# Kernel tuning notes

Measured on AMD Instinct MI355X. Metric: run time of the kernel, lower is better.

Reference implementation:

```python
import jax, jax.numpy as jnp
import numpy as np

STALK_DIM = 16
N_NODES = 50000
N_EDGES = 400000
HIDDEN = 64


def setup_inputs() -> dict:
    key = jax.random.key(0)
    k1, k2, k3, k4 = jax.random.split(key, 4)
    d = STALK_DIM
    x = jax.random.normal(k1, (N_NODES, d), dtype=jnp.float32)
    edge_index = jax.random.randint(k2, (2, N_EDGES), 0, N_NODES, dtype=jnp.int64)
    W1 = jax.random.normal(k3, (HIDDEN, 2 * d), dtype=jnp.float32) * (1.0 / np.sqrt(2 * d))
    b1 = jnp.zeros((HIDDEN,), dtype=jnp.float32)
    W2 = jax.random.normal(k4, (d, HIDDEN), dtype=jnp.float32) * (1.0 / np.sqrt(HIDDEN))
    b2 = jnp.zeros((d,), dtype=jnp.float32)
    return {"x": x, "edge_index": edge_index, "W1": W1, "b1": b1, "W2": W2, "b2": b2}


def reference(x, edge_index, W1, b1, W2, b2):
    d = x.shape[1]
    n = x.shape[0]
    src, dst = edge_index[0], edge_index[1]
    xs, xd = x[src], x[dst]  # [E, d]

    def reflection(a, b):
        h = jax.nn.relu(jnp.concatenate([a, b], axis=1) @ W1.T + b1)
        return h @ W2.T + b2  # [E, d]

    def householder(v):
        # F.normalize(v, dim=1): v / max(||v||, 1e-12)
        vn = v / jnp.maximum(jnp.linalg.norm(v, axis=1, keepdims=True), 1e-12)
        return jnp.eye(d, dtype=v.dtype)[None] - 2.0 * vn[:, :, None] * vn[:, None, :]

    F_s = householder(reflection(xs, xd))  # [E, d, d]
    F_d = householder(reflection(xd, xs))  # [E, d, d]
    L_sd = -jnp.einsum('eki,ekj->eij', F_s, F_d)  # -F_s^T @ F_d, [E, d, d]

    # degrees: both endpoints of every edge contribute 1
    ones_e = jnp.ones(src.shape[0], dtype=x.dtype)
    deg = jnp.zeros(n, dtype=x.dtype).at[src].add(ones_e).at[dst].add(ones_e)
    deg_inv_sqrt = 1.0 / jnp.sqrt(jnp.maximum(deg, 1e-5))
    # D_inv_sqrt is scalar*I per node, so normalization is a scalar coefficient per edge
    coef = deg_inv_sqrt[src] * deg_inv_sqrt[dst]  # [E]

    # out[s] -= D^-1/2_s L D^-1/2_d x[d] ; out[d] -= D^-1/2_d L^T D^-1/2_s x[s]
    msg_s = coef[:, None] * jnp.einsum('eij,ej->ei', L_sd, xd)  # goes to src
    msg_d = coef[:, None] * jnp.einsum('eji,ej->ei', L_sd, xs)  # goes to dst

    out = x - jnp.zeros_like(x).at[src].add(msg_s) - jnp.zeros_like(x).at[dst].add(msg_d)
    return jax.nn.relu(out)
```

## Files before the change

kernel.cpp:

```cpp
#include <hip/hip_runtime.h>
#include <hip/hip_bf16.h>
#include <hip/hip_fp16.h>

#define N_NODES 50000
#define N_EDGES 400000
#define D 16
#define HID 64

#define SCAN_B 256
#define SCAN_G ((N_NODES + SCAN_B - 1) / SCAN_B)

typedef unsigned short ushort_t;
typedef _Float16 h16x2 __attribute__((ext_vector_type(2)));

#define CNT4_OFF  0
#define DEG_OFF   (4 * N_NODES)
#define OFF_OFF   (5 * N_NODES)
#define CUR_OFF   (6 * N_NODES + 1)
#define BS_OFF    (7 * N_NODES + 1)
#define MSG_OFF_I (((BS_OFF + SCAN_G) + 3) & ~3)
#define CSR_NEEDED_BYTES ((size_t)(MSG_OFF_I + 2 * N_EDGES * D) * 4 + 64)

#define FB_NDEG   (N_NODES)
#define FB_NACC   (N_NODES * D)
#define FB_FLAGS  (FB_NDEG + FB_NACC)

__device__ __forceinline__ float bf_bits(ushort_t us) {
    return __uint_as_float(((unsigned)us) << 16);
}
__device__ __forceinline__ float lo_bf(unsigned u) { return __uint_as_float(u << 16); }
__device__ __forceinline__ float hi_bf(unsigned u) { return __uint_as_float(u & 0xffff0000u); }
__device__ __forceinline__ ushort_t f2bf(float v) {
    unsigned u = __float_as_uint(v);
    unsigned r = (u + 0x7fffu + ((u >> 16) & 1u)) >> 16;
    return (ushort_t)r;
}
__device__ __forceinline__ float ld_f(const void* p, int idx, int f32) {
    return f32 ? ((const float*)p)[idx]
               : bf_bits(((const ushort_t*)p)[idx]);
}

__device__ __forceinline__ unsigned pack_h2(float a, float b) {
#if __has_builtin(__builtin_amdgcn_cvt_pkrtz)
    return __builtin_bit_cast(unsigned, __builtin_amdgcn_cvt_pkrtz(a, b));
#else
    h16x2 h;
    h.x = (_Float16)a;
    h.y = (_Float16)b;
    return __builtin_bit_cast(unsigned, h);
#endif
}

#if __has_builtin(__builtin_amdgcn_fdot2)
__device__ __forceinline__ float fdot2u(unsigned a, unsigned b, float c) {
    return __builtin_amdgcn_fdot2(__builtin_bit_cast(h16x2, a),
                                  __builtin_bit_cast(h16x2, b), c, false);
}
#else
__device__ __forceinline__ float fdot2u(unsigned a, unsigned b, float c) {
    h16x2 ha = __builtin_bit_cast(h16x2, a);
    h16x2 hb = __builtin_bit_cast(h16x2, b);
    return fmaf((float)ha.x, (float)hb.x, fmaf((float)ha.y, (float)hb.y, c));
}
#endif

__device__ __forceinline__ void ld16u(const unsigned* __restrict__ p, unsigned* o) {
    const uint4* q = (const uint4*)p;
    uint4 a = q[0], b = q[1], c = q[2], d = q[3];
    o[0]=a.x; o[1]=a.y; o[2]=a.z; o[3]=a.w;
    o[4]=b.x; o[5]=b.y; o[6]=b.z; o[7]=b.w;
    o[8]=c.x; o[9]=c.y; o[10]=c.z; o[11]=c.w;
    o[12]=d.x; o[13]=d.y; o[14]=d.z; o[15]=d.w;
}

__device__ __forceinline__ void load16(const void* __restrict__ p, long long base,
                                       int f32, float* o) {
    if (f32) {
        const float4* q = (const float4*)((const float*)p + base);
        float4 a = q[0], b = q[1], c = q[2], d = q[3];
        o[0]=a.x; o[1]=a.y; o[2]=a.z; o[3]=a.w;
        o[4]=b.x; o[5]=b.y; o[6]=b.z; o[7]=b.w;
        o[8]=c.x; o[9]=c.y; o[10]=c.z; o[11]=c.w;
        o[12]=d.x; o[13]=d.y; o[14]=d.z; o[15]=d.w;
    } else {
        const uint4* q = (const uint4*)((const ushort_t*)p + base);
        uint4 a = q[0], b = q[1];
        unsigned u[8] = {a.x, a.y, a.z, a.w, b.x, b.y, b.z, b.w};
#pragma unroll
        for (int k = 0; k < 8; k++) {
            o[2 * k]     = lo_bf(u[k]);
            o[2 * k + 1] = hi_bf(u[k]);
        }
    }
}

__device__ __forceinline__ void load_edge(const void* __restrict__ ei, int e, int is64,
                                          int& s, int& d) {
    if (is64) {
        const long long* p = (const long long*)ei;
        s = (int)p[e];
        d = (int)p[N_EDGES + e];
    } else {
        const int* p = (const int*)ei;
        s = p[e];
        d = p[N_EDGES + e];
    }
}

__device__ __forceinline__ void detect_flags(const void* x, const void* ei, int* flags) {
    const ushort_t* h = (const ushort_t*)x;
    int f32 = 0;
    for (int k = 0; k < 256; k++) {
        float v = bf_bits(h[k]);
        if (!(v == v) || fabsf(v) > 1.0e6f) { f32 = 1; break; }
    }
    const long long* p = (const long long*)ei;
    int i64 = 1;
    for (int k = 0; k < 16; k++) {
        long long v = p[k];
        if (v < 0 || v >= N_NODES) { i64 = 0; break; }
    }
    flags[0] = f32;
    flags[1] = i64;
}

__device__ __forceinline__ void stage_weights(
    const void* W1, const void* b1, const void* W2, const void* b2, int f32,
    float* sW1, float* sW2t, float* sb1, float* sb2)
{
    int t = threadIdx.x;
    for (int idx = t; idx < HID * 2 * D; idx += blockDim.x)
        sW1[idx] = ld_f(W1, idx, f32);
    for (int idx = t; idx < HID * D; idx += blockDim.x) {
        int j = idx / D, i = idx % D;
        sW2t[idx] = ld_f(W2, i * HID + j, f32);
    }
    if (t < HID) sb1[t] = ld_f(b1, t, f32);
    if (t < D)  sb2[t] = ld_f(b2, t, f32);
}

__device__ __forceinline__ void edge_math_v4(
    const float* __restrict__ sW1, const float* __restrict__ sW2t,
    const float* __restrict__ sb1, const float* __restrict__ sb2,
    const float* xs, const float* xd, float coef,
    float* ms, float* md)
{
    float vs[D], vd[D];
#pragma unroll
    for (int i = 0; i < D; i++) { vs[i] = sb2[i]; vd[i] = sb2[i]; }
#pragma unroll 4
    for (int j = 0; j < HID; j++) {
        float hs = sb1[j], hd = sb1[j];
        const float4* w4 = (const float4*)&sW1[j * 2 * D];
#pragma unroll
        for (int t = 0; t < 4; t++) {
            float4 wv = w4[t];
            int k = 4 * t;
            hs = fmaf(wv.x, xs[k],     hs); hd = fmaf(wv.x, xd[k],     hd);
            hs = fmaf(wv.y, xs[k + 1], hs); hd = fmaf(wv.y, xd[k + 1], hd);
            hs = fmaf(wv.z, xs[k + 2], hs); hd = fmaf(wv.z, xd[k + 2], hd);
            hs = fmaf(wv.w, xs[k + 3], hs); hd = fmaf(wv.w, xd[k + 3], hd);
        }
#pragma unroll
        for (int t = 0; t < 4; t++) {
            float4 wv = w4[4 + t];
            int k = 4 * t;
            hs = fmaf(wv.x, xd[k],     hs); hd = fmaf(wv.x, xs[k],     hd);
            hs = fmaf(wv.y, xd[k + 1], hs); hd = fmaf(wv.y, xs[k + 1], hd);
            hs = fmaf(wv.z, xd[k + 2], hs); hd = fmaf(wv.z, xs[k + 2], hd);
            hs = fmaf(wv.w, xd[k + 3], hs); hd = fmaf(wv.w, xs[k + 3], hd);
        }
        hs = fmaxf(hs, 0.0f);
        hd = fmaxf(hd, 0.0f);
        const float4* w24 = (const float4*)&sW2t[j * D];
#pragma unroll
        for (int t = 0; t < 4; t++) {
            float4 u = w24[t];
            int i = 4 * t;
            vs[i]     = fmaf(u.x, hs, vs[i]);     vd[i]     = fmaf(u.x, hd, vd[i]);
            vs[i + 1] = fmaf(u.y, hs, vs[i + 1]); vd[i + 1] = fmaf(u.y, hd, vd[i + 1]);
            vs[i + 2] = fmaf(u.z, hs, vs[i + 2]); vd[i + 2] = fmaf(u.z, hd, vd[i + 2]);
            vs[i + 3] = fmaf(u.w, hs, vs[i + 3]); vd[i + 3] = fmaf(u.w, hd, vd[i + 3]);
        }
    }
    float ns = 0.0f, nd = 0.0f;
#pragma unroll
    for (int i = 0; i < D; i++) { ns = fmaf(vs[i], vs[i], ns); nd = fmaf(vd[i], vd[i], nd); }
    float is_ = 1.0f / fmaxf(sqrtf(ns), 1e-12f);
    float id_ = 1.0f / fmaxf(sqrtf(nd), 1e-12f);
#pragma unroll
    for (int i = 0; i < D; i++) { vs[i] *= is_; vd[i] *= id_; }
    float dot1 = 0.0f;
#pragma unroll
    for (int i = 0; i < D; i++) dot1 = fmaf(vd[i], xd[i], dot1);
#pragma unroll
    for (int i = 0; i < D; i++) ms[i] = fmaf(-2.0f * dot1, vd[i], xd[i]);
    float dot2 = 0.0f;
#pragma unroll
    for (int i = 0; i < D; i++) dot2 = fmaf(vs[i], ms[i], dot2);
#pragma unroll
    for (int i = 0; i < D; i++) ms[i] = coef * fmaf(-2.0f * dot2, vs[i], ms[i]);
    float dot3 = 0.0f;
#pragma unroll
    for (int i = 0; i < D; i++) dot3 = fmaf(vs[i], xs[i], dot3);
#pragma unroll
    for (int i = 0; i < D; i++) md[i] = fmaf(-2.0f * dot3, vs[i], xs[i]);
    float dot4 = 0.0f;
#pragma unroll
    for (int i = 0; i < D; i++) dot4 = fmaf(vd[i], md[i], dot4);
#pragma unroll
    for (int i = 0; i < D; i++) md[i] = coef * fmaf(-2.0f * dot4, vd[i], md[i]);
}

__global__ void csr_count_kernel(const void* __restrict__ ei,
                                 const void* __restrict__ x,
                                 int* __restrict__ wsI) {
    __shared__ int sfl[2];
    if (threadIdx.x == 0) detect_flags(x, ei, sfl);
    __syncthreads();
    int i64 = sfl[1];
    int e = blockIdx.x * blockDim.x + threadIdx.x;
    if (e >= N_EDGES) return;
    int s, d;
    load_edge(ei, e, i64, s, d);
    int r = (e & 3) * N_NODES;
    atomicAdd(&wsI[CNT4_OFF + r + s], 1);
    atomicAdd(&wsI[CNT4_OFF + r + d], 1);
}

__global__ __launch_bounds__(SCAN_B) void csr_scan1_kernel(int* __restrict__ wsI) {
    __shared__ int sm[SCAN_B];
    int t = threadIdx.x;
    int g = blockIdx.x * SCAN_B + t;
    int c = 0;
    if (g < N_NODES) {
        c = wsI[CNT4_OFF + g] + wsI[CNT4_OFF + N_NODES + g]
          + wsI[CNT4_OFF + 2 * N_NODES + g] + wsI[CNT4_OFF + 3 * N_NODES + g];
        wsI[DEG_OFF + g] = c;
    }
    sm[t] = c;
    __syncthreads();
    for (int st = SCAN_B / 2; st > 0; st >>= 1) {
        if (t < st) sm[t] += sm[t + st];
        __syncthreads();
    }
    if (t == 0) wsI[BS_OFF + blockIdx.x] = sm[0];
}

__global__ __launch_bounds__(SCAN_B) void csr_scan3_kernel(int* __restrict__ wsI) {
    __shared__ int sB[SCAN_B];
    __shared__ int sm[SCAN_B];
    int t = threadIdx.x;
    int bsv = (t < SCAN_G) ? wsI[BS_OFF + t] : 0;
    sB[t] = bsv;
    __syncthreads();
    for (int st = 1; st < SCAN_B; st <<= 1) {
        int u = (t >= st) ? sB[t - st] : 0;
        __syncthreads();
        sB[t] += u;
        __syncthreads();
    }
    int blockBase = sB[blockIdx.x] - wsI[BS_OFF + blockIdx.x];

    int g = blockIdx.x * SCAN_B + t;
    int c = (g < N_NODES) ? wsI[DEG_OFF + g] : 0;
    sm[t] = c;
    __syncthreads();
    for (int st = 1; st < SCAN_B; st <<= 1) {
        int u = (t >= st) ? sm[t - st] : 0;
        __syncthreads();
        sm[t] += u;
        __syncthreads();
    }
    int excl = sm[t] - c + blockBase;
    if (g < N_NODES) {
        wsI[OFF_OFF + g] = excl;
        wsI[CUR_OFF + g] = excl;
        if (g == N_NODES - 1) wsI[OFF_OFF + N_NODES] = excl + c;
    }
}

__global__ __launch_bounds__(256) void csr_edge_kernel(
    const void* __restrict__ x,
    const void* __restrict__ ei,
    const void* __restrict__ W1,
    const void* __restrict__ b1,
    const void* __restrict__ W2,
    const void* __restrict__ b2,
    int* __restrict__ wsI)
{
    __shared__ __align__(16) unsigned sW1h[HID * 16];
    __shared__ __align__(16) unsigned sW2h[32 * 16];
    __shared__ float sb1[HID];
    __shared__ float sb2[D];
    __shared__ __align__(16) float sW1f[HID * 2 * D];
    __shared__ __align__(16) float sW2tf[HID * D];
    __shared__ int sfl[2];

    if (threadIdx.x == 0) detect_flags(x, ei, sfl);
    __syncthreads();
    int f32 = sfl[0], i64 = sfl[1];
    int t = threadIdx.x;

    if (!f32) {
        const ushort_t* W1b = (const ushort_t*)W1;
        for (int idx = t; idx < HID * 16; idx += 256) {
            int j = idx >> 4, tt = idx & 15;
            sW1h[idx] = pack_h2(bf_bits(W1b[j * 32 + 2 * tt]),
                                bf_bits(W1b[j * 32 + 2 * tt + 1]));
        }
        const ushort_t* W2b = (const ushort_t*)W2;
        for (int idx = t; idx < 32 * 16; idx += 256) {
            int jj = idx >> 4, i = idx & 15;
            sW2h[idx] = pack_h2(bf_bits(W2b[i * HID + 2 * jj]),
                                bf_bits(W2b[i * HID + 2 * jj + 1]));
        }
    } else {
        for (int idx = t; idx < HID * 2 * D; idx += 256)
            sW1f[idx] = ld_f(W1, idx, 1);
        for (int idx = t; idx < HID * D; idx += 256) {
            int j = idx / D, i = idx % D;
            sW2tf[idx] = ld_f(W2, i * HID + j, 1);
        }
    }
    if (t < HID) sb1[t] = ld_f(b1, t, f32);
    if (t < D)  sb2[t] = ld_f(b2, t, f32);
    __syncthreads();

    int e = blockIdx.x * 256 + t;
    if (e >= N_EDGES) return;

    int s, d;
    load_edge(ei, e, i64, s, d);
    float degs = (float)wsI[DEG_OFF + s];
    float degd = (float)wsI[DEG_OFF + d];
    float coef = (1.0f / sqrtf(fmaxf(degs, 1e-5f))) * (1.0f / sqrtf(fmaxf(degd, 1e-5f)));
    float* msg = (float*)(wsI + MSG_OFF_I);

    if (!f32) {
        unsigned xsh[8], xdh[8];
        {
            const uint4* q = (const uint4*)((const ushort_t*)x + (long long)s * D);
            uint4 a = q[0], b = q[1];
            unsigned u[8] = {a.x, a.y, a.z, a.w, b.x, b.y, b.z, b.w};
#pragma unroll
            for (int k = 0; k < 8; k++) xsh[k] = pack_h2(lo_bf(u[k]), hi_bf(u[k]));
        }
        {
            const uint4* q = (const uint4*)((const ushort_t*)x + (long long)d * D);
            uint4 a = q[0], b = q[1];
            unsigned u[8] = {a.x, a.y, a.z, a.w, b.x, b.y, b.z, b.w};
#pragma unroll
            for (int k = 0; k < 8; k++) xdh[k] = pack_h2(lo_bf(u[k]), hi_bf(u[k]));
        }

        float vs[D], vd[D];
#pragma unroll
        for (int i = 0; i < D; i++) { vs[i] = sb2[i]; vd[i] = sb2[i]; }

#pragma unroll 2
        for (int jj = 0; jj < 32; jj++) {
            unsigned wr[32];
            ld16u(&sW1h[(2 * jj) * 16], wr);
            ld16u(&sW1h[(2 * jj) * 16 + 16], wr + 16);
            unsigned w2r[16];
            ld16u(&sW2h[jj * 16], w2r);

            float hs0 = sb1[2 * jj],     hd0 = hs0;
            float hs1 = sb1[2 * jj + 1], hd1 = hs1;
#pragma unroll
            for (int k = 0; k < 8; k++) {
                hs0 = fdot2u(wr[k],      xsh[k], hs0);
                hd0 = fdot2u(wr[k],      xdh[k], hd0);
                hs1 = fdot2u(wr[16 + k], xsh[k], hs1);
                hd1 = fdot2u(wr[16 + k], xdh[k], hd1);
            }
#pragma unroll
            for (int k = 0; k < 8; k++) {
                hs0 = fdot2u(wr[8 + k],  xdh[k], hs0);
                hd0 = fdot2u(wr[8 + k],  xsh[k], hd0);
                hs1 = fdot2u(wr[24 + k], xdh[k], hs1);
                hd1 = fdot2u(wr[24 + k], xsh[k], hd1);
            }
            hs0 = fmaxf(hs0, 0.0f); hd0 = fmaxf(hd0, 0.0f);
            hs1 = fmaxf(hs1, 0.0f); hd1 = fmaxf(hd1, 0.0f);
            unsigned hsp = pack_h2(hs0, hs1);
            unsigned hdp = pack_h2(hd0, hd1);
#pragma unroll
            for (int i = 0; i < D; i++) {
                vs[i] = fdot2u(w2r[i], hsp, vs[i]);
                vd[i] = fdot2u(w2r[i], hdp, vd[i]);
            }
        }

        float xs[D], xd[D];
#pragma unroll
        for (int k = 0; k < 8; k++) {
            h16x2 a = __builtin_bit_cast(h16x2, xsh[k]);
            xs[2 * k] = (float)a.x; xs[2 * k + 1] = (float)a.y;
            h16x2 b = __builtin_bit_cast(h16x2, xdh[k]);
            xd[2 * k] = (float)b.x; xd[2 * k + 1] = (float)b.y;
        }

        float ns = 0.0f, nd = 0.0f;
#pragma unroll
        for (int i = 0; i < D; i++) { ns = fmaf(vs[i], vs[i], ns); nd = fmaf(vd[i], vd[i], nd); }
        float is_ = 1.0f / fmaxf(sqrtf(ns), 1e-12f);
        float id_ = 1.0f / fmaxf(sqrtf(nd), 1e-12f);
#pragma unroll
        for (int i = 0; i < D; i++) { vs[i] *= is_; vd[i] *= id_; }

        float ms[D], md[D];
        float dot1 = 0.0f;
#pragma unroll
        for (int i = 0; i < D; i++) dot1 = fmaf(vd[i], xd[i], dot1);
#pragma unroll
        for (int i = 0; i < D; i++) ms[i] = fmaf(-2.0f * dot1, vd[i], xd[i]);
        float dot2 = 0.0f;
#pragma unroll
        for (int i = 0; i < D; i++) dot2 = fmaf(vs[i], ms[i], dot2);
#pragma unroll
        for (int i = 0; i < D; i++) ms[i] = coef * fmaf(-2.0f * dot2, vs[i], ms[i]);
        float dot3 = 0.0f;
#pragma unroll
        for (int i = 0; i < D; i++) dot3 = fmaf(vs[i], xs[i], dot3);
#pragma unroll
        for (int i = 0; i < D; i++) md[i] = fmaf(-2.0f * dot3, vs[i], xs[i]);
        float dot4 = 0.0f;
#pragma unroll
        for (int i = 0; i < D; i++) dot4 = fmaf(vd[i], md[i], dot4);
#pragma unroll
        for (int i = 0; i < D; i++) md[i] = coef * fmaf(-2.0f * dot4, vd[i], md[i]);

        int slot_s = atomicAdd(&wsI[CUR_OFF + s], 1);
        float4* m0 = (float4*)(msg + (long long)slot_s * D);
        m0[0] = make_float4(ms[0], ms[1], ms[2], ms[3]);
        m0[1] = make_float4(ms[4], ms[5], ms[6], ms[7]);
        m0[2] = make_float4(ms[8], ms[9], ms[10], ms[11]);
        m0[3] = make_float4(ms[12], ms[13], ms[14], ms[15]);
        int slot_d = atomicAdd(&wsI[CUR_OFF + d], 1);
        float4* m1 = (float4*)(msg + (long long)slot_d * D);
        m1[0] = make_float4(md[0], md[1], md[2], md[3]);
        m1[1] = make_float4(md[4], md[5], md[6], md[7]);
        m1[2] = make_float4(md[8], md[9], md[10], md[11]);
        m1[3] = make_float4(md[12], md[13], md[14], md[15]);
    } else {
        float xs[D], xd[D];
        load16(x, (long long)s * D, 1, xs);
        load16(x, (long long)d * D, 1, xd);
        float ms[D], md[D];
        edge_math_v4(sW1f, sW2tf, sb1, sb2, xs, xd, coef, ms, md);
        int slot_s = atomicAdd(&wsI[CUR_OFF + s], 1);
        float4* m0 = (float4*)(msg + (long long)slot_s * D);
        m0[0] = make_float4(ms[0], ms[1], ms[2], ms[3]);
        m0[1] = make_float4(ms[4], ms[5], ms[6], ms[7]);
        m0[2] = make_float4(ms[8], ms[9], ms[10], ms[11]);
        m0[3] = make_float4(ms[12], ms[13], ms[14], ms[15]);
        int slot_d = atomicAdd(&wsI[CUR_OFF + d], 1);
        float4* m1 = (float4*)(msg + (long long)slot_d * D);
        m1[0] = make_float4(md[0], md[1], md[2], md[3]);
        m1[1] = make_float4(md[4], md[5], md[6], md[7]);
        m1[2] = make_float4(md[8], md[9], md[10], md[11]);
        m1[3] = make_float4(md[12], md[13], md[14], md[15]);
    }
}

__global__ __launch_bounds__(256) void csr_gather_kernel(
    const void* __restrict__ x,
    const void* __restrict__ ei,
    const int* __restrict__ wsI,
    void* __restrict__ out)
{
    __shared__ int sfl[2];
    if (threadIdx.x == 0) detect_flags(x, ei, sfl);
    __syncthreads();
    int f32 = sfl[0];

    int n = blockIdx.x * 64 + (threadIdx.x >> 2);
    int c = threadIdx.x & 3;
    if (n >= N_NODES) return;

    const int* off = wsI + OFF_OFF;
    const float4* msg4 = (const float4*)(wsI + MSG_OFF_I);

    int beg = off[n], end = off[n + 1];
    float4 a = make_float4(0.0f, 0.0f, 0.0f, 0.0f);
    int it = beg;
    for (; it + 2 <= end; it += 2) {
        float4 u = msg4[(long long)it * 4 + c];
        float4 v = msg4[(long long)(it + 1) * 4 + c];
        a.x += u.x + v.x; a.y += u.y + v.y; a.z += u.z + v.z; a.w += u.w + v.w;
    }
    if (it < end) {
        float4 u = msg4[(long long)it * 4 + c];
        a.x += u.x; a.y += u.y; a.z += u.z; a.w += u.w;
    }

    long long xb = (long long)n * D + 4 * c;
    float4 xv;
    if (f32) {
        xv = *(const float4*)((const float*)x + xb);
    } else {
        uint2 u = *(const uint2*)((const ushort_t*)x + xb);
        xv.x = lo_bf(u.x); xv.y = hi_bf(u.x);
        xv.z = lo_bf(u.y); xv.w = hi_bf(u.y);
    }
    float4 r;
    r.x = fmaxf(xv.x + a.x, 0.0f);
    r.y = fmaxf(xv.y + a.y, 0.0f);
    r.z = fmaxf(xv.z + a.z, 0.0f);
    r.w = fmaxf(xv.w + a.w, 0.0f);
    if (f32) {
        *(float4*)((float*)out + xb) = r;
    } else {
        uint2 o;
        o.x = (unsigned)f2bf(r.x) | ((unsigned)f2bf(r.y) << 16);
        o.y = (unsigned)f2bf(r.z) | ((unsigned)f2bf(r.w) << 16);
        *(uint2*)((ushort_t*)out + xb) = o;
    }
}

__global__ void fb_init_kernel(float* __restrict__ ws,
                               const void* __restrict__ x,
                               const void* __restrict__ ei) {
    int i = blockIdx.x * blockDim.x + threadIdx.x;
    if (i < FB_FLAGS) ws[i] = 0.0f;
    if (blockIdx.x == 0 && threadIdx.x == 0)
        detect_flags(x, ei, (int*)(ws + FB_FLAGS));
}

__global__ void fb_deg_kernel(const void* __restrict__ ei, float* __restrict__ ws) {
    int i64 = ((const int*)(ws + FB_FLAGS))[1];
    int e = blockIdx.x * blockDim.x + threadIdx.x;
    if (e >= N_EDGES) return;
    int s, d;
    load_edge(ei, e, i64, s, d);
    atomicAdd(&ws[s], 1.0f);
    atomicAdd(&ws[d], 1.0f);
}

__global__ __launch_bounds__(256) void fb_edge_kernel(
    const void* __restrict__ x, const void* __restrict__ ei,
    const void* __restrict__ W1, const void* __restrict__ b1,
    const void* __restrict__ W2, const void* __restrict__ b2,
    float* __restrict__ ws)
{
    __shared__ __align__(16) float sW1[HID * 2 * D];
    __shared__ __align__(16) float sW2t[HID * D];
    __shared__ float sb1[HID];
    __shared__ float sb2[D];
    const int* flags = (const int*)(ws + FB_FLAGS);
    int f32 = flags[0], i64 = flags[1];
    stage_weights(W1, b1, W2, b2, f32, sW1, sW2t, sb1, sb2);
    __syncthreads();
    int e = blockIdx.x * blockDim.x + threadIdx.x;
    if (e >= N_EDGES) return;
    int s, d;
    load_edge(ei, e, i64, s, d);
    float xs[D], xd[D];
    load16(x, (long long)s * D, f32, xs);
    load16(x, (long long)d * D, f32, xd);
    float coef = (1.0f / sqrtf(fmaxf(ws[s], 1e-5f))) * (1.0f / sqrtf(fmaxf(ws[d], 1e-5f)));
    float ms[D], md[D];
    edge_math_v4(sW1, sW2t, sb1, sb2, xs, xd, coef, ms, md);
    float* acc = ws + FB_NDEG;
#pragma unroll
    for (int i = 0; i < D; i++) atomicAdd(&acc[(long long)s * D + i], ms[i]);
#pragma unroll
    for (int i = 0; i < D; i++) atomicAdd(&acc[(long long)d * D + i], md[i]);
}

__global__ void fb_finalize_kernel(const void* __restrict__ x,
                                   const float* __restrict__ ws,
                                   void* __restrict__ out)
{
    int f32 = ((const int*)(ws + FB_FLAGS))[0];
    const float* acc = ws + FB_NDEG;
    int i = blockIdx.x * blockDim.x + threadIdx.x;
    if (i >= FB_NACC) return;
    float v = ld_f(x, i, f32) + acc[i];
    v = fmaxf(v, 0.0f);
    if (f32) ((float*)out)[i] = v;
    else     ((__hip_bfloat16*)out)[i] = __float2bfloat16(v);
}

extern "C" void kernel_launch(void* const* d_in, const int* in_sizes, int n_in,
                              void* d_out, int out_size, void* d_ws, size_t ws_size,
                              hipStream_t stream)
{
    const void* x  = d_in[0];
    const void* ei = d_in[1];
    const void* W1 = d_in[2];
    const void* b1 = d_in[3];
    const void* W2 = d_in[4];
    const void* b2 = d_in[5];

    int blk = 256;
    if (ws_size >= CSR_NEEDED_BYTES) {
        int* wsI = (int*)d_ws;
        hipMemsetAsync(d_ws, 0, (size_t)4 * N_NODES * sizeof(int), stream);
        csr_count_kernel<<<(N_EDGES + blk - 1) / blk, blk, 0, stream>>>(ei, x, wsI);
        csr_scan1_kernel<<<SCAN_G, SCAN_B, 0, stream>>>(wsI);
        csr_scan3_kernel<<<SCAN_G, SCAN_B, 0, stream>>>(wsI);
        csr_edge_kernel<<<(N_EDGES + blk - 1) / blk, blk, 0, stream>>>(x, ei, W1, b1, W2, b2, wsI);
        csr_gather_kernel<<<(N_NODES + 63) / 64, blk, 0, stream>>>(x, ei, wsI, d_out);
    } else {
        float* ws = (float*)d_ws;
        fb_init_kernel<<<(FB_FLAGS + blk - 1) / blk, blk, 0, stream>>>(ws, x, ei);
        fb_deg_kernel<<<(N_EDGES + blk - 1) / blk, blk, 0, stream>>>(ei, ws);
        fb_edge_kernel<<<(N_EDGES + blk - 1) / blk, blk, 0, stream>>>(x, ei, W1, b1, W2, b2, ws);
        fb_finalize_kernel<<<(FB_NACC + blk - 1) / blk, blk, 0, stream>>>(x, ws, d_out);
    }
}
```

Before: 200.0 us.

## Compute per-edge MLP with MFMA matrix instructions in bf16 path

Replaces the per-thread fdot2-based two-layer MLP in the bf16 path with wave-level MFMA: each wave processes 64 edges in 16-edge groups, computing hidden activations with bf16 MFMA and the output layer with f16 MFMA via an LDS staging buffer. Weights are held in registers per lane instead of shared memory. The Householder math and message scatter stay per-thread, reading MLP outputs back from LDS. This adds LDS traffic and precision changes (bf16 first layer inputs) in exchange for much higher arithmetic throughput.

```diff
diff --git a/kernel.cpp b/kernel.cpp
--- a/kernel.cpp
+++ b/kernel.cpp
@@ -12,6 +12,9 @@
 
 typedef unsigned short ushort_t;
 typedef _Float16 h16x2 __attribute__((ext_vector_type(2)));
+typedef __attribute__((ext_vector_type(8))) short bf16x8_t;
+typedef __attribute__((ext_vector_type(8))) _Float16 f16x8_t;
+typedef __attribute__((ext_vector_type(4))) float f32x4_t;
 
 #define CNT4_OFF  0
 #define DEG_OFF   (4 * N_NODES)
@@ -24,6 +27,12 @@
 #define FB_NDEG   (N_NODES)
 #define FB_NACC   (N_NODES * D)
 #define FB_FLAGS  (FB_NDEG + FB_NACC)
+
+#define HSTRIDE 80
+#define VSTRIDE 36
+#define WAVE_H_BYTES (16 * HSTRIDE * 2)
+#define WAVE_V_BYTES (64 * VSTRIDE * 4)
+#define WAVE_LDS (WAVE_H_BYTES + WAVE_V_BYTES)
 
 __device__ __forceinline__ float bf_bits(ushort_t us) {
     return __uint_as_float(((unsigned)us) << 16);
@@ -49,28 +58,6 @@
     h.y = (_Float16)b;
     return __builtin_bit_cast(unsigned, h);
 #endif
-}
-
-#if __has_builtin(__builtin_amdgcn_fdot2)
-__device__ __forceinline__ float fdot2u(unsigned a, unsigned b, float c) {
-    return __builtin_amdgcn_fdot2(__builtin_bit_cast(h16x2, a),
-                                  __builtin_bit_cast(h16x2, b), c, false);
-}
-#else
-__device__ __forceinline__ float fdot2u(unsigned a, unsigned b, float c) {
-    h16x2 ha = __builtin_bit_cast(h16x2, a);
-    h16x2 hb = __builtin_bit_cast(h16x2, b);
-    return fmaf((float)ha.x, (float)hb.x, fmaf((float)ha.y, (float)hb.y, c));
-}
-#endif
-
-__device__ __forceinline__ void ld16u(const unsigned* __restrict__ p, unsigned* o) {
-    const uint4* q = (const uint4*)p;
-    uint4 a = q[0], b = q[1], c = q[2], d = q[3];
-    o[0]=a.x; o[1]=a.y; o[2]=a.z; o[3]=a.w;
-    o[4]=b.x; o[5]=b.y; o[6]=b.z; o[7]=b.w;
-    o[8]=c.x; o[9]=c.y; o[10]=c.z; o[11]=c.w;
-    o[12]=d.x; o[13]=d.y; o[14]=d.z; o[15]=d.w;
 }
 
 __device__ __forceinline__ void load16(const void* __restrict__ p, long long base,
@@ -289,162 +276,36 @@
     const void* __restrict__ b2,
     int* __restrict__ wsI)
 {
-    __shared__ __align__(16) unsigned sW1h[HID * 16];
-    __shared__ __align__(16) unsigned sW2h[32 * 16];
-    __shared__ float sb1[HID];
-    __shared__ float sb2[D];
-    __shared__ __align__(16) float sW1f[HID * 2 * D];
-    __shared__ __align__(16) float sW2tf[HID * D];
+    __shared__ __align__(16) char smem[4 * WAVE_LDS];
     __shared__ int sfl[2];
-
     if (threadIdx.x == 0) detect_flags(x, ei, sfl);
     __syncthreads();
     int f32 = sfl[0], i64 = sfl[1];
     int t = threadIdx.x;
-
-    if (!f32) {
-        const ushort_t* W1b = (const ushort_t*)W1;
-        for (int idx = t; idx < HID * 16; idx += 256) {
-            int j = idx >> 4, tt = idx & 15;
-            sW1h[idx] = pack_h2(bf_bits(W1b[j * 32 + 2 * tt]),
-                                bf_bits(W1b[j * 32 + 2 * tt + 1]));
-        }
-        const ushort_t* W2b = (const ushort_t*)W2;
-        for (int idx = t; idx < 32 * 16; idx += 256) {
-            int jj = idx >> 4, i = idx & 15;
-            sW2h[idx] = pack_h2(bf_bits(W2b[i * HID + 2 * jj]),
-                                bf_bits(W2b[i * HID + 2 * jj + 1]));
-        }
-    } else {
+    float* msg = (float*)(wsI + MSG_OFF_I);
+
+    if (f32) {
+        float* sW1f  = (float*)smem;
+        float* sW2tf = sW1f + HID * 2 * D;
+        float* sb1   = sW2tf + HID * D;
+        float* sb2   = sb1 + HID;
         for (int idx = t; idx < HID * 2 * D; idx += 256)
-            sW1f[idx] = ld_f(W1, idx, 1);
+            sW1f[idx] = ((const float*)W1)[idx];
         for (int idx = t; idx < HID * D; idx += 256) {
             int j = idx / D, i = idx % D;
-            sW2tf[idx] = ld_f(W2, i * HID + j, 1);
-        }
-    }
-    if (t < HID) sb1[t] = ld_f(b1, t, f32);
-    if (t < D)  sb2[t] = ld_f(b2, t, f32);
-    __syncthreads();
-
-    int e = blockIdx.x * 256 + t;
-    if (e >= N_EDGES) return;
-
-    int s, d;
-    load_edge(ei, e, i64, s, d);
-    float degs = (float)wsI[DEG_OFF + s];
-    float degd = (float)wsI[DEG_OFF + d];
-    float coef = (1.0f / sqrtf(fmaxf(degs, 1e-5f))) * (1.0f / sqrtf(fmaxf(degd, 1e-5f)));
-    float* msg = (float*)(wsI + MSG_OFF_I);
-
-    if (!f32) {
-        unsigned xsh[8], xdh[8];
-        {
-            const uint4* q = (const uint4*)((const ushort_t*)x + (long long)s * D);
-            uint4 a = q[0], b = q[1];
-            unsigned u[8] = {a.x, a.y, a.z, a.w, b.x, b.y, b.z, b.w};
-#pragma unroll
-            for (int k = 0; k < 8; k++) xsh[k] = pack_h2(lo_bf(u[k]), hi_bf(u[k]));
-        }
-        {
-            const uint4* q = (const uint4*)((const ushort_t*)x + (long long)d * D);
-            uint4 a = q[0], b = q[1];
-            unsigned u[8] = {a.x, a.y, a.z, a.w, b.x, b.y, b.z, b.w};
-#pragma unroll
-            for (int k = 0; k < 8; k++) xdh[k] = pack_h2(lo_bf(u[k]), hi_bf(u[k]));
-        }
-
-        float vs[D], vd[D];
-#pragma unroll
-        for (int i = 0; i < D; i++) { vs[i] = sb2[i]; vd[i] = sb2[i]; }
-
-#pragma unroll 2
-        for (int jj = 0; jj < 32; jj++) {
-            unsigned wr[32];
-            ld16u(&sW1h[(2 * jj) * 16], wr);
-            ld16u(&sW1h[(2 * jj) * 16 + 16], wr + 16);
-            unsigned w2r[16];
-            ld16u(&sW2h[jj * 16], w2r);
-
-            float hs0 = sb1[2 * jj],     hd0 = hs0;
-            float hs1 = sb1[2 * jj + 1], hd1 = hs1;
-#pragma unroll
-            for (int k = 0; k < 8; k++) {
-                hs0 = fdot2u(wr[k],      xsh[k], hs0);
-                hd0 = fdot2u(wr[k],      xdh[k], hd0);
-                hs1 = fdot2u(wr[16 + k], xsh[k], hs1);
-                hd1 = fdot2u(wr[16 + k], xdh[k], hd1);
-            }
-#pragma unroll
-            for (int k = 0; k < 8; k++) {
-                hs0 = fdot2u(wr[8 + k],  xdh[k], hs0);
-                hd0 = fdot2u(wr[8 + k],  xsh[k], hd0);
-                hs1 = fdot2u(wr[24 + k], xdh[k], hs1);
-                hd1 = fdot2u(wr[24 + k], xsh[k], hd1);
-            }
-            hs0 = fmaxf(hs0, 0.0f); hd0 = fmaxf(hd0, 0.0f);
-            hs1 = fmaxf(hs1, 0.0f); hd1 = fmaxf(hd1, 0.0f);
-            unsigned hsp = pack_h2(hs0, hs1);
-            unsigned hdp = pack_h2(hd0, hd1);
-#pragma unroll
-            for (int i = 0; i < D; i++) {
-                vs[i] = fdot2u(w2r[i], hsp, vs[i]);
-                vd[i] = fdot2u(w2r[i], hdp, vd[i]);
-            }
-        }
-
-        float xs[D], xd[D];
-#pragma unroll
-        for (int k = 0; k < 8; k++) {
-            h16x2 a = __builtin_bit_cast(h16x2, xsh[k]);
-            xs[2 * k] = (float)a.x; xs[2 * k + 1] = (float)a.y;
-            h16x2 b = __builtin_bit_cast(h16x2, xdh[k]);
-            xd[2 * k] = (float)b.x; xd[2 * k + 1] = (float)b.y;
-        }
-
-        float ns = 0.0f, nd = 0.0f;
-#pragma unroll
-        for (int i = 0; i < D; i++) { ns = fmaf(vs[i], vs[i], ns); nd = fmaf(vd[i], vd[i], nd); }
-        float is_ = 1.0f / fmaxf(sqrtf(ns), 1e-12f);
-        float id_ = 1.0f / fmaxf(sqrtf(nd), 1e-12f);
-#pragma unroll
-        for (int i = 0; i < D; i++) { vs[i] *= is_; vd[i] *= id_; }
-
-        float ms[D], md[D];
-        float dot1 = 0.0f;
-#pragma unroll
-        for (int i = 0; i < D; i++) dot1 = fmaf(vd[i], xd[i], dot1);
-#pragma unroll
-        for (int i = 0; i < D; i++) ms[i] = fmaf(-2.0f * dot1, vd[i], xd[i]);
-        float dot2 = 0.0f;
-#pragma unroll
-        for (int i = 0; i < D; i++) dot2 = fmaf(vs[i], ms[i], dot2);
-#pragma unroll
-        for (int i = 0; i < D; i++) ms[i] = coef * fmaf(-2.0f * dot2, vs[i], ms[i]);
-        float dot3 = 0.0f;
-#pragma unroll
-        for (int i = 0; i < D; i++) dot3 = fmaf(vs[i], xs[i], dot3);
-#pragma unroll
-        for (int i = 0; i < D; i++) md[i] = fmaf(-2.0f * dot3, vs[i], xs[i]);
-        float dot4 = 0.0f;
-#pragma unroll
-        for (int i = 0; i < D; i++) dot4 = fmaf(vd[i], md[i], dot4);
-#pragma unroll
-        for (int i = 0; i < D; i++) md[i] = coef * fmaf(-2.0f * dot4, vd[i], md[i]);
-
-        int slot_s = atomicAdd(&wsI[CUR_OFF + s], 1);
-        float4* m0 = (float4*)(msg + (long long)slot_s * D);
-        m0[0] = make_float4(ms[0], ms[1], ms[2], ms[3]);
-        m0[1] = make_float4(ms[4], ms[5], ms[6], ms[7]);
-        m0[2] = make_float4(ms[8], ms[9], ms[10], ms[11]);
-        m0[3] = make_float4(ms[12], ms[13], ms[14], ms[15]);
-        int slot_d = atomicAdd(&wsI[CUR_OFF + d], 1);
-        float4* m1 = (float4*)(msg + (long long)slot_d * D);
-        m1[0] = make_float4(md[0], md[1], md[2], md[3]);
-        m1[1] = make_float4(md[4], md[5], md[6], md[7]);
-        m1[2] = make_float4(md[8], md[9], md[10], md[11]);
-        m1[3] = make_float4(md[12], md[13], md[14], md[15]);
-    } else {
+            sW2tf[idx] = ((const float*)W2)[i * HID + j];
+        }
+        if (t < HID) sb1[t] = ((const float*)b1)[t];
+        if (t < D)  sb2[t] = ((const float*)b2)[t];
+        __syncthreads();
+
+        int e = blockIdx.x * 256 + t;
+        if (e >= N_EDGES) return;
+        int s, d;
+        load_edge(ei, e, i64, s, d);
+        float degs = (float)wsI[DEG_OFF + s];
+        float degd = (float)wsI[DEG_OFF + d];
+        float coef = (1.0f / sqrtf(fmaxf(degs, 1e-5f))) * (1.0f / sqrtf(fmaxf(degd, 1e-5f)));
         float xs[D], xd[D];
         load16(x, (long long)s * D, 1, xs);
         load16(x, (long long)d * D, 1, xd);
@@ -462,7 +323,169 @@
         m1[1] = make_float4(md[4], md[5], md[6], md[7]);
         m1[2] = make_float4(md[8], md[9], md[10], md[11]);
         m1[3] = make_float4(md[12], md[13], md[14], md[15]);
-    }
+        return;
+    }
+
+    const int wave = t >> 6;
+    const int lane = t & 63;
+    const int g4 = lane >> 4;
+    const int c  = lane & 15;
+    const int ebase = blockIdx.x * 256 + wave * 64;
+    if (ebase >= N_EDGES) return;
+
+    char* wbase = smem + wave * WAVE_LDS;
+    _Float16* hw = (_Float16*)wbase;
+    float* vbuf = (float*)(wbase + WAVE_H_BYTES);
+
+    const ushort_t* xb  = (const ushort_t*)x;
+    const ushort_t* W1b = (const ushort_t*)W1;
+    const ushort_t* W2b = (const ushort_t*)W2;
+    const ushort_t* b1b = (const ushort_t*)b1;
+    const ushort_t* b2b = (const ushort_t*)b2;
+
+    bf16x8_t B1[4], B1s[4];
+#pragma unroll
+    for (int tt = 0; tt < 4; tt++) {
+        B1[tt]  = *(const bf16x8_t*)(W1b + (16 * tt + c) * (2 * D) + g4 * 8);
+        B1s[tt] = *(const bf16x8_t*)(W1b + (16 * tt + c) * (2 * D) + ((g4 ^ 2) * 8));
+    }
+    f16x8_t B2[2];
+#pragma unroll
+    for (int q = 0; q < 2; q++) {
+        const ushort_t* p = W2b + c * HID + q * 32 + g4 * 8;
+        uint4 raw = *(const uint4*)p;
+        unsigned u[4] = {raw.x, raw.y, raw.z, raw.w};
+        f16x8_t hv;
+#pragma unroll
+        for (int k = 0; k < 4; k++) {
+            hv[2 * k]     = (_Float16)lo_bf(u[k]);
+            hv[2 * k + 1] = (_Float16)hi_bf(u[k]);
+        }
+        B2[q] = hv;
+    }
+    float b1c[4];
+#pragma unroll
+    for (int tt = 0; tt < 4; tt++) b1c[tt] = bf_bits(b1b[16 * tt + c]);
+    float b2c = bf_bits(b2b[c]);
+
+#pragma unroll 1
+    for (int G = 0; G < 4; G++) {
+        const int e0 = ebase + G * 16;
+        int nid = 0;
+        if (lane < 32) {
+            int idx = (lane < 16) ? (e0 + lane) : (N_EDGES + e0 + lane - 16);
+            nid = i64 ? (int)((const long long*)ei)[idx] : ((const int*)ei)[idx];
+        }
+        int an = __shfl(nid, (g4 < 2) ? c : (c + 16), 64);
+        bf16x8_t A1 = *(const bf16x8_t*)(xb + (long long)an * D + (g4 & 1) * 8);
+
+        f32x4_t cs[4], cd[4];
+#pragma unroll
+        for (int tt = 0; tt < 4; tt++) {
+            f32x4_t bi = {b1c[tt], b1c[tt], b1c[tt], b1c[tt]};
+            cs[tt] = __builtin_amdgcn_mfma_f32_16x16x32_bf16(A1, B1[tt],  bi, 0, 0, 0);
+            cd[tt] = __builtin_amdgcn_mfma_f32_16x16x32_bf16(A1, B1s[tt], bi, 0, 0, 0);
+        }
+
+#pragma unroll
+        for (int tt = 0; tt < 4; tt++)
+#pragma unroll
+            for (int r = 0; r < 4; r++)
+                hw[(g4 * 4 + r) * HSTRIDE + 16 * tt + c] = (_Float16)fmaxf(cs[tt][r], 0.0f);
+        f32x4_t vS = {b2c, b2c, b2c, b2c};
+#pragma unroll
+        for (int q = 0; q < 2; q++) {
+            f16x8_t a2 = *(const f16x8_t*)(hw + c * HSTRIDE + q * 32 + g4 * 8);
+            vS = __builtin_amdgcn_mfma_f32_16x16x32_f16(a2, B2[q], vS, 0, 0, 0);
+        }
+#pragma unroll
+        for (int r = 0; r < 4; r++)
+            vbuf[(G * 16 + g4 * 4 + r) * VSTRIDE + c] = vS[r];
+
+#pragma unroll
+        for (int tt = 0; tt < 4; tt++)
+#pragma unroll
+            for (int r = 0; r < 4; r++)
+                hw[(g4 * 4 + r) * HSTRIDE + 16 * tt + c] = (_Float16)fmaxf(cd[tt][r], 0.0f);
+        f32x4_t vD = {b2c, b2c, b2c, b2c};
+#pragma unroll
+        for (int q = 0; q < 2; q++) {
+            f16x8_t a2 = *(const f16x8_t*)(hw + c * HSTRIDE + q * 32 + g4 * 8);
+            vD = __builtin_amdgcn_mfma_f32_16x16x32_f16(a2, B2[q], vD, 0, 0, 0);
+        }
+#pragma unroll
+        for (int r = 0; r < 4; r++)
+            vbuf[(G * 16 + g4 * 4 + r) * VSTRIDE + 16 + c] = vD[r];
+    }
+
+    int e = ebase + lane;
+    int s, d;
+    load_edge(ei, e, i64, s, d);
+    float degs = (float)wsI[DEG_OFF + s];
+    float degd = (float)wsI[DEG_OFF + d];
+    float coef = (1.0f / sqrtf(fmaxf(degs, 1e-5f))) * (1.0f / sqrtf(fmaxf(degd, 1e-5f)));
+
+    float vs[D], vd[D];
+    {
+        const f32x4_t* vp = (const f32x4_t*)(vbuf + lane * VSTRIDE);
+#pragma unroll
+        for (int i = 0; i < 4; i++) {
+            f32x4_t u = vp[i];
+            vs[4 * i] = u[0]; vs[4 * i + 1] = u[1]; vs[4 * i + 2] = u[2]; vs[4 * i + 3] = u[3];
+        }
+        const f32x4_t* vq = (const f32x4_t*)(vbuf + lane * VSTRIDE + 16);
+#pragma unroll
+        for (int i = 0; i < 4; i++) {
+            f32x4_t u = vq[i];
+            vd[4 * i] = u[0]; vd[4 * i + 1] = u[1]; vd[4 * i + 2] = u[2]; vd[4 * i + 3] = u[3];
+        }
+    }
+    float xs[D], xd[D];
+    load16(x, (long long)s * D, 0, xs);
+    load16(x, (long long)d * D, 0, xd);
+
+    float ns = 0.0f, nd = 0.0f;
+#pragma unroll
+    for (int i = 0; i < D; i++) { ns = fmaf(vs[i], vs[i], ns); nd = fmaf(vd[i], vd[i], nd); }
+    float is_ = 1.0f / fmaxf(sqrtf(ns), 1e-12f);
+    float id_ = 1.0f / fmaxf(sqrtf(nd), 1e-12f);
+#pragma unroll
+    for (int i = 0; i < D; i++) { vs[i] *= is_; vd[i] *= id_; }
+
+    float ms[D], md[D];
+    float dot1 = 0.0f;
+#pragma unroll
+    for (int i = 0; i < D; i++) dot1 = fmaf(vd[i], xd[i], dot1);
+#pragma unroll
+    for (int i = 0; i < D; i++) ms[i] = fmaf(-2.0f * dot1, vd[i], xd[i]);
+    float dot2 = 0.0f;
+#pragma unroll
+    for (int i = 0; i < D; i++) dot2 = fmaf(vs[i], ms[i], dot2);
+#pragma unroll
+    for (int i = 0; i < D; i++) ms[i] = coef * fmaf(-2.0f * dot2, vs[i], ms[i]);
+    float dot3 = 0.0f;
+#pragma unroll
+    for (int i = 0; i < D; i++) dot3 = fmaf(vs[i], xs[i], dot3);
+#pragma unroll
+    for (int i = 0; i < D; i++) md[i] = fmaf(-2.0f * dot3, vs[i], xs[i]);
+    float dot4 = 0.0f;
+#pragma unroll
+    for (int i = 0; i < D; i++) dot4 = fmaf(vd[i], md[i], dot4);
+#pragma unroll
+    for (int i = 0; i < D; i++) md[i] = coef * fmaf(-2.0f * dot4, vd[i], md[i]);
+
+    int slot_s = atomicAdd(&wsI[CUR_OFF + s], 1);
+    float4* m0 = (float4*)(msg + (long long)slot_s * D);
+    m0[0] = make_float4(ms[0], ms[1], ms[2], ms[3]);
+    m0[1] = make_float4(ms[4], ms[5], ms[6], ms[7]);
+    m0[2] = make_float4(ms[8], ms[9], ms[10], ms[11]);
+    m0[3] = make_float4(ms[12], ms[13], ms[14], ms[15]);
+    int slot_d = atomicAdd(&wsI[CUR_OFF + d], 1);
+    float4* m1 = (float4*)(msg + (long long)slot_d * D);
+    m1[0] = make_float4(md[0], md[1], md[2], md[3]);
+    m1[1] = make_float4(md[4], md[5], md[6], md[7]);
+    m1[2] = make_float4(md[8], md[9], md[10], md[11]);
+    m1[3] = make_float4(md[12], md[13], md[14], md[15]);
 }
 
 __global__ __launch_bounds__(256) void csr_gather_kernel(
```

After: 220.8 us. 1.1x slower.

## Prepack bf16 weights once in count kernel, read from global in edge kernel

Applied to the files above, without the earlier changes.

Block 0 of the count kernel now converts W1, W2, b1 and b2 from bf16 into packed fp16 pairs and fp32 biases, laid out per hidden pair, and writes them to a workspace region. The edge kernel's bf16 path no longer stages weights into shared memory per block and skips the __syncthreads, loading each 52-dword chunk straight from global/L2 as uniform vector loads with unroll 1. This removes per-block conversion and LDS traffic, and the smaller LDS footprint may raise occupancy, at the cost of global loads in the inner loop. The f32 path is unchanged.

```diff
diff --git a/kernel.cpp b/kernel.cpp
--- a/kernel.cpp
+++ b/kernel.cpp
@@ -19,7 +19,9 @@
 #define CUR_OFF   (6 * N_NODES + 1)
 #define BS_OFF    (7 * N_NODES + 1)
 #define MSG_OFF_I (((BS_OFF + SCAN_G) + 3) & ~3)
-#define CSR_NEEDED_BYTES ((size_t)(MSG_OFF_I + 2 * N_EDGES * D) * 4 + 64)
+#define PREP_OFF  (MSG_OFF_I + 2 * N_EDGES * D)
+#define PREP_DW   (32 * 52 + 16)
+#define CSR_NEEDED_BYTES ((size_t)(PREP_OFF + PREP_DW) * 4 + 64)
 
 #define FB_NDEG   (N_NODES)
 #define FB_NACC   (N_NODES * D)
@@ -63,15 +65,6 @@
     return fmaf((float)ha.x, (float)hb.x, fmaf((float)ha.y, (float)hb.y, c));
 }
 #endif
-
-__device__ __forceinline__ void ld16u(const unsigned* __restrict__ p, unsigned* o) {
-    const uint4* q = (const uint4*)p;
-    uint4 a = q[0], b = q[1], c = q[2], d = q[3];
-    o[0]=a.x; o[1]=a.y; o[2]=a.z; o[3]=a.w;
-    o[4]=b.x; o[5]=b.y; o[6]=b.z; o[7]=b.w;
-    o[8]=c.x; o[9]=c.y; o[10]=c.z; o[11]=c.w;
-    o[12]=d.x; o[13]=d.y; o[14]=d.z; o[15]=d.w;
-}
 
 __device__ __forceinline__ void load16(const void* __restrict__ p, long long base,
                                        int f32, float* o) {
@@ -214,11 +207,44 @@
 
 __global__ void csr_count_kernel(const void* __restrict__ ei,
                                  const void* __restrict__ x,
+                                 const void* __restrict__ W1,
+                                 const void* __restrict__ b1,
+                                 const void* __restrict__ W2,
+                                 const void* __restrict__ b2,
                                  int* __restrict__ wsI) {
     __shared__ int sfl[2];
     if (threadIdx.x == 0) detect_flags(x, ei, sfl);
     __syncthreads();
     int i64 = sfl[1];
+
+    if (blockIdx.x == 0) {
+        unsigned* pp = (unsigned*)(wsI + PREP_OFF);
+        const ushort_t* W1b = (const ushort_t*)W1;
+        const ushort_t* W2b = (const ushort_t*)W2;
+        const ushort_t* b1b = (const ushort_t*)b1;
+        const ushort_t* b2b = (const ushort_t*)b2;
+        for (int idx = threadIdx.x; idx < 32 * 52; idx += 256) {
+            int jj = idx / 52, w = idx % 52;
+            unsigned val = 0;
+            if (w < 32) {
+                int row = 2 * jj + (w >> 4), k2 = w & 15;
+                val = pack_h2(bf_bits(W1b[row * 32 + 2 * k2]),
+                              bf_bits(W1b[row * 32 + 2 * k2 + 1]));
+            } else if (w < 48) {
+                int i = w - 32;
+                val = pack_h2(bf_bits(W2b[i * HID + 2 * jj]),
+                              bf_bits(W2b[i * HID + 2 * jj + 1]));
+            } else if (w == 48) {
+                val = __float_as_uint(bf_bits(b1b[2 * jj]));
+            } else if (w == 49) {
+                val = __float_as_uint(bf_bits(b1b[2 * jj + 1]));
+            }
+            pp[idx] = val;
+        }
+        if (threadIdx.x < D)
+            pp[32 * 52 + threadIdx.x] = __float_as_uint(bf_bits(b2b[threadIdx.x]));
+    }
+
     int e = blockIdx.x * blockDim.x + threadIdx.x;
     if (e >= N_EDGES) return;
     int s, d;
@@ -287,14 +313,13 @@
     const void* __restrict__ b1,
     const void* __restrict__ W2,
     const void* __restrict__ b2,
+    const unsigned* __restrict__ prep,
     int* __restrict__ wsI)
 {
-    __shared__ __align__(16) unsigned sW1h[HID * 16];
-    __shared__ __align__(16) unsigned sW2h[32 * 16];
+    __shared__ __align__(16) float sW1f[HID * 2 * D];
+    __shared__ __align__(16) float sW2tf[HID * D];
     __shared__ float sb1[HID];
     __shared__ float sb2[D];
-    __shared__ __align__(16) float sW1f[HID * 2 * D];
-    __shared__ __align__(16) float sW2tf[HID * D];
     __shared__ int sfl[2];
 
     if (threadIdx.x == 0) detect_flags(x, ei, sfl);
@@ -302,30 +327,17 @@
     int f32 = sfl[0], i64 = sfl[1];
     int t = threadIdx.x;
 
-    if (!f32) {
-        const ushort_t* W1b = (const ushort_t*)W1;
-        for (int idx = t; idx < HID * 16; idx += 256) {
-            int j = idx >> 4, tt = idx & 15;
-            sW1h[idx] = pack_h2(bf_bits(W1b[j * 32 + 2 * tt]),
-                                bf_bits(W1b[j * 32 + 2 * tt + 1]));
-        }
-        const ushort_t* W2b = (const ushort_t*)W2;
-        for (int idx = t; idx < 32 * 16; idx += 256) {
-            int jj = idx >> 4, i = idx & 15;
-            sW2h[idx] = pack_h2(bf_bits(W2b[i * HID + 2 * jj]),
-                                bf_bits(W2b[i * HID + 2 * jj + 1]));
-        }
-    } else {
+    if (f32) {
         for (int idx = t; idx < HID * 2 * D; idx += 256)
             sW1f[idx] = ld_f(W1, idx, 1);
         for (int idx = t; idx < HID * D; idx += 256) {
             int j = idx / D, i = idx % D;
             sW2tf[idx] = ld_f(W2, i * HID + j, 1);
         }
-    }
-    if (t < HID) sb1[t] = ld_f(b1, t, f32);
-    if (t < D)  sb2[t] = ld_f(b2, t, f32);
-    __syncthreads();
+        if (t < HID) sb1[t] = ld_f(b1, t, 1);
+        if (t < D)  sb2[t] = ld_f(b2, t, 1);
+        __syncthreads();
+    }
 
     int e = blockIdx.x * 256 + t;
     if (e >= N_EDGES) return;
@@ -354,33 +366,40 @@
             for (int k = 0; k < 8; k++) xdh[k] = pack_h2(lo_bf(u[k]), hi_bf(u[k]));
         }
 
+        const float* b2f = (const float*)(prep + 32 * 52);
         float vs[D], vd[D];
 #pragma unroll
-        for (int i = 0; i < D; i++) { vs[i] = sb2[i]; vd[i] = sb2[i]; }
-
-#pragma unroll 2
+        for (int i = 0; i < D; i++) { vs[i] = b2f[i]; vd[i] = b2f[i]; }
+
+#pragma unroll 1
         for (int jj = 0; jj < 32; jj++) {
-            unsigned wr[32];
-            ld16u(&sW1h[(2 * jj) * 16], wr);
-            ld16u(&sW1h[(2 * jj) * 16 + 16], wr + 16);
-            unsigned w2r[16];
-            ld16u(&sW2h[jj * 16], w2r);
-
-            float hs0 = sb1[2 * jj],     hd0 = hs0;
-            float hs1 = sb1[2 * jj + 1], hd1 = hs1;
+            const uint4* wb = (const uint4*)(prep + jj * 52);
+            uint4 q0 = wb[0], q1 = wb[1], q2 = wb[2], q3 = wb[3];
+            uint4 q4 = wb[4], q5 = wb[5], q6 = wb[6], q7 = wb[7];
+            uint4 q8 = wb[8], q9 = wb[9], qA = wb[10], qB = wb[11];
+            const float* bb = (const float*)(prep + jj * 52 + 48);
+            float hs0 = bb[0], hd0 = bb[0];
+            float hs1 = bb[1], hd1 = bb[1];
+
+            unsigned r0[16] = {q0.x, q0.y, q0.z, q0.w, q1.x, q1.y, q1.z, q1.w,
+                               q2.x, q2.y, q2.z, q2.w, q3.x, q3.y, q3.z, q3.w};
+            unsigned r1[16] = {q4.x, q4.y, q4.z, q4.w, q5.x, q5.y, q5.z, q5.w,
+                               q6.x, q6.y, q6.z, q6.w, q7.x, q7.y, q7.z, q7.w};
+            unsigned w2a[16] = {q8.x, q8.y, q8.z, q8.w, q9.x, q9.y, q9.z, q9.w,
+                                qA.x, qA.y, qA.z, qA.w, qB.x, qB.y, qB.z, qB.w};
 #pragma unroll
             for (int k = 0; k < 8; k++) {
-                hs0 = fdot2u(wr[k],      xsh[k], hs0);
-                hd0 = fdot2u(wr[k],      xdh[k], hd0);
-                hs1 = fdot2u(wr[16 + k], xsh[k], hs1);
-                hd1 = fdot2u(wr[16 + k], xdh[k], hd1);
+                hs0 = fdot2u(r0[k], xsh[k], hs0);
+                hd0 = fdot2u(r0[k], xdh[k], hd0);
+                hs1 = fdot2u(r1[k], xsh[k], hs1);
+                hd1 = fdot2u(r1[k], xdh[k], hd1);
             }
 #pragma unroll
             for (int k = 0; k < 8; k++) {
-                hs0 = fdot2u(wr[8 + k],  xdh[k], hs0);
-                hd0 = fdot2u(wr[8 + k],  xsh[k], hd0);
-                hs1 = fdot2u(wr[24 + k], xdh[k], hs1);
-                hd1 = fdot2u(wr[24 + k], xsh[k], hd1);
+                hs0 = fdot2u(r0[8 + k], xdh[k], hs0);
+                hd0 = fdot2u(r0[8 + k], xsh[k], hd0);
+                hs1 = fdot2u(r1[8 + k], xdh[k], hs1);
+                hd1 = fdot2u(r1[8 + k], xsh[k], hd1);
             }
             hs0 = fmaxf(hs0, 0.0f); hd0 = fmaxf(hd0, 0.0f);
             hs1 = fmaxf(hs1, 0.0f); hd1 = fmaxf(hd1, 0.0f);
@@ -388,8 +407,8 @@
             unsigned hdp = pack_h2(hd0, hd1);
 #pragma unroll
             for (int i = 0; i < D; i++) {
-                vs[i] = fdot2u(w2r[i], hsp, vs[i]);
-                vd[i] = fdot2u(w2r[i], hdp, vd[i]);
+                vs[i] = fdot2u(w2a[i], hsp, vs[i]);
+                vd[i] = fdot2u(w2a[i], hdp, vd[i]);
             }
         }
 
@@ -599,10 +618,11 @@
     if (ws_size >= CSR_NEEDED_BYTES) {
         int* wsI = (int*)d_ws;
         hipMemsetAsync(d_ws, 0, (size_t)4 * N_NODES * sizeof(int), stream);
-        csr_count_kernel<<<(N_EDGES + blk - 1) / blk, blk, 0, stream>>>(ei, x, wsI);
+        csr_count_kernel<<<(N_EDGES + blk - 1) / blk, blk, 0, stream>>>(ei, x, W1, b1, W2, b2, wsI);
         csr_scan1_kernel<<<SCAN_G, SCAN_B, 0, stream>>>(wsI);
         csr_scan3_kernel<<<SCAN_G, SCAN_B, 0, stream>>>(wsI);
-        csr_edge_kernel<<<(N_EDGES + blk - 1) / blk, blk, 0, stream>>>(x, ei, W1, b1, W2, b2, wsI);
+        csr_edge_kernel<<<(N_EDGES + blk - 1) / blk, blk, 0, stream>>>(
+            x, ei, W1, b1, W2, b2, (const unsigned*)(wsI + PREP_OFF), wsI);
         csr_gather_kernel<<<(N_NODES + 63) / 64, blk, 0, stream>>>(x, ei, wsI, d_out);
     } else {
         float* ws = (float*)d_ws;
```

After: 205.9 us. 3.0% more time.
